# Kernel tuning notes

Hardware: AMD Instinct MI355X
Metric: run time of the kernel (lower is better)

Reference implementation:

```python
import jax, jax.numpy as jnp
import numpy as np

B, F, NP, DIM, H, DH = 4, 16, 196, 512, 8, 64  # batch, frames, patches, dim, heads, dim_head
N = 1 + F * NP  # sequence length incl CLS


def setup_inputs() -> dict:
    key = jax.random.key(0)
    k1, k2, k3, k4 = jax.random.split(key, 4)
    return {
        "x": jax.random.normal(k1, (B, N, DIM), dtype=jnp.float32),
        "W_qkv": jax.random.normal(k2, (DIM, 3 * H * DH), dtype=jnp.float32) * 0.05,
        "W_out": jax.random.normal(k3, (H * DH, DIM), dtype=jnp.float32) * 0.05,
        "b_out": jax.random.normal(k4, (DIM,), dtype=jnp.float32) * 0.05,
        "f": F,
    }


def _attn(q, k, v):
    # q: [bb, i, d], k/v: [bb, j, d]
    sim = jnp.einsum('bid,bjd->bij', q, k)
    a = jax.nn.softmax(sim, axis=-1)
    return jnp.einsum('bij,bjd->bid', a, v)


def reference(x, W_qkv, W_out, b_out, f):
    b, n_tot, dim = x.shape
    h, d = H, DH
    scale = d ** (-0.5)
    qkv = x @ W_qkv  # [b, N, 3*h*d]
    q, k, v = jnp.split(qkv, 3, axis=-1)

    def to_bh(t):  # b n (h d) -> (b h) n d
        return t.reshape(b, n_tot, h, d).transpose(0, 2, 1, 3).reshape(b * h, n_tot, d)

    q, k, v = map(to_bh, (q, k, v))
    q = q * scale

    cls_q, q_ = q[:, :1], q[:, 1:]
    cls_k, k_ = k[:, :1], k[:, 1:]
    cls_v, v_ = v[:, :1], v[:, 1:]

    # CLS token attends over the full sequence
    cls_out = _attn(cls_q, k, v)  # [(b h), 1, d]

    # spatial factorization: (b h) (f n) d -> (b h f) n d
    n = (n_tot - 1) // f
    def split_f(t):
        return t.reshape(b * h * f, n, d)
    q_, k_, v_ = map(split_f, (q_, k_, v_))

    # repeat CLS k/v per frame: b () d -> (b r) () d with r = f
    cls_k_r = jnp.repeat(cls_k, f, axis=0)
    cls_v_r = jnp.repeat(cls_v, f, axis=0)
    k_ = jnp.concatenate([cls_k_r, k_], axis=1)  # [(b h f), n+1, d]
    v_ = jnp.concatenate([cls_v_r, v_], axis=1)

    out = _attn(q_, k_, v_)  # [(b h f), n, d]
    out = out.reshape(b * h, f * n, d)
    out = jnp.concatenate([cls_out, out], axis=1)  # [(b h), N, d]
    out = out.reshape(b, h, n_tot, d).transpose(0, 2, 1, 3).reshape(b, n_tot, h * d)
    return out @ W_out + b_out
```

## Files before the change

kernel.cpp:

```cpp
#include <hip/hip_runtime.h>
#include <math.h>

#define B_   4
#define F_   16
#define NP_  196
#define DIM_ 512
#define H_   8
#define DH_  64
#define NTOT 3137
#define BH_  32
#define MROWS 12548
#define QSZ_ ((size_t)BH_ * NTOT * DH_)
#define KVPAD 224
#define PSTRIDE 232
#define NCHUNK 13

typedef unsigned short u16;
typedef __attribute__((ext_vector_type(8))) short    bf16x8;
typedef __attribute__((ext_vector_type(8))) unsigned short u16x8;
typedef __attribute__((ext_vector_type(4))) unsigned short u16x4;
typedef __attribute__((ext_vector_type(4))) float    f32x4;

__device__ __forceinline__ u16 f2bf(float f) {
    unsigned int u = __float_as_uint(f);
    unsigned int r = (u + 0x7FFFu + ((u >> 16) & 1u)) >> 16;
    return (u16)r;
}
__device__ __forceinline__ float bf2f(u16 u) {
    return __uint_as_float(((unsigned int)u) << 16);
}

__device__ __forceinline__ void gl2lds16(const u16* g, u16* l) {
    __builtin_amdgcn_global_load_lds(
        (const __attribute__((address_space(1))) unsigned int*)(g),
        (__attribute__((address_space(3))) unsigned int*)(l),
        16, 0, 0);
}

__global__ __launch_bounds__(256) void convert_x_kernel(
    const float* __restrict__ x, u16* __restrict__ xbf)
{
    int idx = blockIdx.x * 256 + threadIdx.x;
    float4 v = ((const float4*)x)[idx];
    u16x4 p = { f2bf(v.x), f2bf(v.y), f2bf(v.z), f2bf(v.w) };
    *(u16x4*)(&xbf[(size_t)idx * 4]) = p;
}

__global__ __launch_bounds__(256) void transpose_bf16_kernel(
    const float* __restrict__ src, u16* __restrict__ dst, int R, int C)
{
    __shared__ float t[32][33];
    const int tx = threadIdx.x & 31, ty = threadIdx.x >> 5;
    const int c0 = blockIdx.x * 32, r0 = blockIdx.y * 32;
    #pragma unroll
    for (int i = 0; i < 4; ++i) {
        int r = ty + i * 8;
        t[r][tx] = src[(size_t)(r0 + r) * C + c0 + tx];
    }
    __syncthreads();
    #pragma unroll
    for (int i = 0; i < 4; ++i) {
        int cc = ty + i * 8;
        dst[(size_t)(c0 + cc) * R + r0 + tx] = f2bf(t[tx][cc]);
    }
}

template<int MODE>
__global__ __launch_bounds__(256) void gemm_bf16_mfma(
    const u16* __restrict__ A, const u16* __restrict__ BT,
    u16* __restrict__ Cq, u16* __restrict__ Ck, u16* __restrict__ Cv,
    u16* __restrict__ CvT, float* __restrict__ Cout, const float* __restrict__ bias)
{
    __shared__ alignas(16) u16 Asm[8 * 512];
    __shared__ alignas(16) u16 Bsm[8 * 512];

    const int tid  = threadIdx.x;
    const int wave = tid >> 6, lane = tid & 63;
    const int wr = wave >> 1, wc = wave & 1;
    const int lm = lane & 15, lq = lane >> 4;
    const int row0 = blockIdx.y * 128;
    const int col0 = blockIdx.x * 128;

    f32x4 acc[4][4];
    #pragma unroll
    for (int i = 0; i < 4; ++i)
        #pragma unroll
        for (int j = 0; j < 4; ++j) acc[i][j] = (f32x4){0.f, 0.f, 0.f, 0.f};

    for (int k0 = 0; k0 < 512; k0 += 32) {
        #pragma unroll
        for (int i = 0; i < 2; ++i) {
            int s = wave * 2 + i;
            int arow = row0 + s * 16 + lm;
            if (arow >= MROWS) arow = MROWS - 1;
            gl2lds16(A + (size_t)arow * 512 + k0 + lq * 8, &Asm[s * 512 + lane * 8]);
            int brow = col0 + s * 16 + lm;
            gl2lds16(BT + (size_t)brow * 512 + k0 + lq * 8, &Bsm[s * 512 + lane * 8]);
        }
        __syncthreads();
        bf16x8 af[4], bf[4];
        #pragma unroll
        for (int mi = 0; mi < 4; ++mi)
            af[mi] = *(const bf16x8*)(&Asm[(wr * 4 + mi) * 512 + lane * 8]);
        #pragma unroll
        for (int ni = 0; ni < 4; ++ni)
            bf[ni] = *(const bf16x8*)(&Bsm[(wc * 4 + ni) * 512 + lane * 8]);
        #pragma unroll
        for (int mi = 0; mi < 4; ++mi)
            #pragma unroll
            for (int ni = 0; ni < 4; ++ni)
                acc[mi][ni] = __builtin_amdgcn_mfma_f32_16x16x32_bf16(
                    af[mi], bf[ni], acc[mi][ni], 0, 0, 0);
        __syncthreads();
    }

    if (MODE == 0) {
        const int t3 = col0 >> 9;
        #pragma unroll
        for (int mi = 0; mi < 4; ++mi) {
            #pragma unroll
            for (int r = 0; r < 4; ++r) {
                int gr = row0 + wr * 64 + mi * 16 + lq * 4 + r;
                if (gr >= MROWS) continue;
                int b = gr / NTOT;
                int n = gr - b * NTOT;
                #pragma unroll
                for (int ni = 0; ni < 4; ++ni) {
                    int gc = col0 + wc * 64 + ni * 16 + lm;
                    int rem = gc & 511;
                    int h = rem >> 6, d = rem & 63;
                    int bh = b * H_ + h;
                    size_t tok = (size_t)bh * NTOT + n;
                    float v = acc[mi][ni][r];
                    if (t3 == 0) {
                        Cq[tok * 64 + d] = f2bf(v * 0.125f);
                    } else if (t3 == 1) {
                        Ck[tok * 64 + d] = f2bf(v);
                    } else {
                        u16 bv = f2bf(v);
                        Cv[tok * 64 + d] = bv;
                        if (n > 0) {
                            unsigned nn = (unsigned)(n - 1);
                            unsigned f = nn / 196u;
                            unsigned jj = nn - f * 196u + 1u;
                            CvT[((size_t)(bh * 16 + (int)f) * 64 + d) * KVPAD + jj] = bv;
                        }
                    }
                }
            }
        }
    } else {
        float bb[4];
        #pragma unroll
        for (int ni = 0; ni < 4; ++ni)
            bb[ni] = bias[col0 + wc * 64 + ni * 16 + lm];
        #pragma unroll
        for (int mi = 0; mi < 4; ++mi) {
            #pragma unroll
            for (int r = 0; r < 4; ++r) {
                int gr = row0 + wr * 64 + mi * 16 + lq * 4 + r;
                if (gr >= MROWS) continue;
                #pragma unroll
                for (int ni = 0; ni < 4; ++ni) {
                    int gc = col0 + wc * 64 + ni * 16 + lm;
                    Cout[(size_t)gr * 512 + gc] = acc[mi][ni][r] + bb[ni];
                }
            }
        }
    }
}

__global__ __launch_bounds__(64) void vt_cls_fill_kernel(
    const u16* __restrict__ vb, u16* __restrict__ vT)
{
    const int bh = blockIdx.x, d = threadIdx.x;
    u16 val = vb[(size_t)bh * NTOT * 64 + d];
    #pragma unroll
    for (int f = 0; f < 16; ++f)
        vT[((size_t)(bh * 16 + f) * 64 + d) * KVPAD] = val;
}

__global__ __launch_bounds__(256) void attn_mfma_kernel(
    const u16* __restrict__ qb, const u16* __restrict__ kb,
    const u16* __restrict__ vT, u16* __restrict__ attn)
{
    __shared__ alignas(16) u16 Pbuf[4 * 16 * PSTRIDE];

    const int tid  = threadIdx.x;
    const int wave = tid >> 6, lane = tid & 63;
    const int lm = lane & 15, lq = lane >> 4;
    const int task = blockIdx.x * 4 + wave;
    const int mt = task % 13;
    const int gf = task / 13;
    const int f  = gf & 15;
    const int bh = gf >> 4;

    const int rq = min(mt * 16 + lm, 195);
    const u16* qrow = qb + ((size_t)bh * NTOT + (1 + f * NP_ + rq)) * 64;
    bf16x8 qf0 = *(const bf16x8*)(qrow + lq * 8);
    bf16x8 qf1 = *(const bf16x8*)(qrow + 32 + lq * 8);

    f32x4 S[13];
    #pragma unroll
    for (int nt = 0; nt < 13; ++nt) {
        int rkc = min(nt * 16 + lm, 196);
        int nk = (rkc == 0) ? 0 : (1 + f * NP_ + rkc - 1);
        const u16* krow = kb + ((size_t)bh * NTOT + nk) * 64;
        bf16x8 kf0 = *(const bf16x8*)(krow + lq * 8);
        bf16x8 kf1 = *(const bf16x8*)(krow + 32 + lq * 8);
        f32x4 z = (f32x4){0.f, 0.f, 0.f, 0.f};
        z = __builtin_amdgcn_mfma_f32_16x16x32_bf16(qf0, kf0, z, 0, 0, 0);
        z = __builtin_amdgcn_mfma_f32_16x16x32_bf16(qf1, kf1, z, 0, 0, 0);
        S[nt] = z;
    }

    #pragma unroll
    for (int nt = 0; nt < 13; ++nt)
        if (nt * 16 + lm >= 197) {
            S[nt][0] = -INFINITY; S[nt][1] = -INFINITY;
            S[nt][2] = -INFINITY; S[nt][3] = -INFINITY;
        }

    float invl[4];
    #pragma unroll
    for (int r = 0; r < 4; ++r) {
        float mx = -INFINITY;
        #pragma unroll
        for (int nt = 0; nt < 13; ++nt) mx = fmaxf(mx, S[nt][r]);
        mx = fmaxf(mx, __shfl_xor(mx, 1, 64));
        mx = fmaxf(mx, __shfl_xor(mx, 2, 64));
        mx = fmaxf(mx, __shfl_xor(mx, 4, 64));
        mx = fmaxf(mx, __shfl_xor(mx, 8, 64));
        float sum = 0.f;
        #pragma unroll
        for (int nt = 0; nt < 13; ++nt) {
            float p = __expf(S[nt][r] - mx);
            S[nt][r] = p;
            sum += p;
        }
        sum += __shfl_xor(sum, 1, 64);
        sum += __shfl_xor(sum, 2, 64);
        sum += __shfl_xor(sum, 4, 64);
        sum += __shfl_xor(sum, 8, 64);
        invl[r] = 1.f / sum;
    }

    u16* P = Pbuf + wave * 16 * PSTRIDE;
    #pragma unroll
    for (int nt = 0; nt < 13; ++nt) {
        int col = nt * 16 + lm;
        #pragma unroll
        for (int r = 0; r < 4; ++r)
            P[(lq * 4 + r) * PSTRIDE + col] = f2bf(S[nt][r]);
    }
    {
        u16x4 z4 = {0, 0, 0, 0};
        *(u16x4*)(P + lm * PSTRIDE + 208 + lq * 4) = z4;
    }

    f32x4 O[4];
    #pragma unroll
    for (int nd = 0; nd < 4; ++nd) O[nd] = (f32x4){0.f, 0.f, 0.f, 0.f};
    const u16* vbase = vT + (size_t)(bh * 16 + f) * 64 * KVPAD;
    #pragma unroll
    for (int ks = 0; ks < 7; ++ks) {
        bf16x8 pf = *(const bf16x8*)(P + lm * PSTRIDE + ks * 32 + lq * 8);
        #pragma unroll
        for (int nd = 0; nd < 4; ++nd) {
            bf16x8 vf = *(const bf16x8*)(vbase + (size_t)(nd * 16 + lm) * KVPAD + ks * 32 + lq * 8);
            O[nd] = __builtin_amdgcn_mfma_f32_16x16x32_bf16(pf, vf, O[nd], 0, 0, 0);
        }
    }

    const int b = bh >> 3, h = bh & 7;
    #pragma unroll
    for (int r = 0; r < 4; ++r) {
        int rql = mt * 16 + lq * 4 + r;
        if (rql >= 196) continue;
        int n = 1 + f * NP_ + rql;
        u16* dst = attn + ((size_t)b * NTOT + n) * 512 + h * 64;
        float s = invl[r];
        #pragma unroll
        for (int nd = 0; nd < 4; ++nd)
            dst[nd * 16 + lm] = f2bf(O[nd][r] * s);
    }
}

__global__ __launch_bounds__(256) void attn_cls_partial_kernel(
    const u16* __restrict__ qb, const u16* __restrict__ kb,
    const u16* __restrict__ vb, float* __restrict__ cls_m,
    float* __restrict__ cls_l, float* __restrict__ cls_o)
{
    __shared__ float qs[64];
    __shared__ float redm[4], redl[4];
    __shared__ float ps[256];
    __shared__ float so[4][64];

    const int c = blockIdx.x, bh = blockIdx.y;
    const int t = threadIdx.x;
    const int lane = t & 63, w = t >> 6;

    if (t < 64) qs[t] = bf2f(qb[(size_t)bh * NTOT * 64 + t]);
    __syncthreads();

    const int j = c * 256 + t;
    const bool valid = (j < NTOT);
    const int jc = valid ? j : (NTOT - 1);
    const u16* krow = kb + ((size_t)bh * NTOT + jc) * 64;
    float s0 = 0.f, s1 = 0.f, s2 = 0.f, s3 = 0.f;
    #pragma unroll
    for (int i = 0; i < 8; ++i) {
        u16x8 k8 = *(const u16x8*)(krow + i * 8);
        const float* qp = qs + i * 8;
        s0 = fmaf(qp[0], bf2f(k8[0]), s0);
        s1 = fmaf(qp[1], bf2f(k8[1]), s1);
        s2 = fmaf(qp[2], bf2f(k8[2]), s2);
        s3 = fmaf(qp[3], bf2f(k8[3]), s3);
        s0 = fmaf(qp[4], bf2f(k8[4]), s0);
        s1 = fmaf(qp[5], bf2f(k8[5]), s1);
        s2 = fmaf(qp[6], bf2f(k8[6]), s2);
        s3 = fmaf(qp[7], bf2f(k8[7]), s3);
    }
    float s = (s0 + s1) + (s2 + s3);
    if (!valid) s = -INFINITY;

    float mx = s;
    #pragma unroll
    for (int off = 1; off < 64; off <<= 1) mx = fmaxf(mx, __shfl_xor(mx, off, 64));
    if (lane == 0) redm[w] = mx;
    __syncthreads();
    mx = fmaxf(fmaxf(redm[0], redm[1]), fmaxf(redm[2], redm[3]));

    float pv = __expf(s - mx);
    float l = pv;
    #pragma unroll
    for (int off = 1; off < 64; off <<= 1) l += __shfl_xor(l, off, 64);
    if (lane == 0) redl[w] = l;
    ps[t] = pv;
    __syncthreads();
    l = redl[0] + redl[1] + redl[2] + redl[3];

    const int d = lane, part = w;
    float o = 0.f;
    #pragma unroll 8
    for (int i = 0; i < 64; ++i) {
        int jj = c * 256 + part * 64 + i;
        int jjc = (jj < NTOT) ? jj : (NTOT - 1);
        o = fmaf(ps[part * 64 + i], bf2f(vb[((size_t)bh * NTOT + jjc) * 64 + d]), o);
    }
    so[part][d] = o;
    __syncthreads();
    if (t < 64) {
        float O = so[0][t] + so[1][t] + so[2][t] + so[3][t];
        int pi = bh * NCHUNK + c;
        cls_o[(size_t)pi * 64 + t] = O;
        if (t == 0) { cls_m[pi] = mx; cls_l[pi] = l; }
    }
}

__global__ __launch_bounds__(64) void attn_cls_merge_kernel(
    const float* __restrict__ cls_m, const float* __restrict__ cls_l,
    const float* __restrict__ cls_o, u16* __restrict__ attn)
{
    const int bh = blockIdx.x, lane = threadIdx.x;
    float M = -INFINITY;
    #pragma unroll
    for (int p = 0; p < NCHUNK; ++p) M = fmaxf(M, cls_m[bh * NCHUNK + p]);
    float L = 0.f, O = 0.f;
    #pragma unroll
    for (int p = 0; p < NCHUNK; ++p) {
        float al = __expf(cls_m[bh * NCHUNK + p] - M);
        L += cls_l[bh * NCHUNK + p] * al;
        O += cls_o[(size_t)(bh * NCHUNK + p) * 64 + lane] * al;
    }
    const int b = bh >> 3, h = bh & 7;
    attn[(size_t)b * NTOT * 512 + h * 64 + lane] = f2bf(O / L);
}

extern "C" void kernel_launch(void* const* d_in, const int* in_sizes, int n_in,
                              void* d_out, int out_size, void* d_ws, size_t ws_size,
                              hipStream_t stream) {
    const float* x    = (const float*)d_in[0];
    const float* wqkv = (const float*)d_in[1];
    const float* wout = (const float*)d_in[2];
    const float* bout = (const float*)d_in[3];

    u16* p = (u16*)d_ws;
    u16* xbf   = p;                    p += (size_t)MROWS * 512;
    u16* attn  = xbf;
    u16* wqkvT = p;                    p += (size_t)1536 * 512;
    u16* woutT = p;                    p += (size_t)512 * 512;
    u16* qbuf  = p;                    p += QSZ_;
    u16* kbuf  = p;                    p += QSZ_;
    u16* vbuf  = p;                    p += QSZ_;
    u16* vT    = p;                    p += (size_t)BH_ * 16 * 64 * KVPAD;
    float* clsws = (float*)p;
    float* cls_m = clsws;
    float* cls_l = clsws + BH_ * NCHUNK;
    float* cls_o = clsws + 2 * BH_ * NCHUNK;
    float* outp  = (float*)d_out;

    convert_x_kernel<<<6274, 256, 0, stream>>>(x, xbf);
    transpose_bf16_kernel<<<dim3(48, 16), 256, 0, stream>>>(wqkv, wqkvT, 512, 1536);
    transpose_bf16_kernel<<<dim3(16, 16), 256, 0, stream>>>(wout, woutT, 512, 512);
    gemm_bf16_mfma<0><<<dim3(12, 99), 256, 0, stream>>>(
        xbf, wqkvT, qbuf, kbuf, vbuf, vT, nullptr, nullptr);
    vt_cls_fill_kernel<<<32, 64, 0, stream>>>(vbuf, vT);
    attn_mfma_kernel<<<1664, 256, 0, stream>>>(qbuf, kbuf, vT, attn);
    attn_cls_partial_kernel<<<dim3(NCHUNK, 32), 256, 0, stream>>>(
        qbuf, kbuf, vbuf, cls_m, cls_l, cls_o);
    attn_cls_merge_kernel<<<32, 64, 0, stream>>>(cls_m, cls_l, cls_o, attn);
    gemm_bf16_mfma<1><<<dim3(4, 99), 256, 0, stream>>>(
        attn, woutT, nullptr, nullptr, nullptr, nullptr, outp, bout);
}
```

Measured before the change: 227.3 us.

## Double-buffer GEMM LDS staging, enlarge QKV tile, build transposed V separately

```diff
diff --git a/kernel.cpp b/kernel.cpp
--- a/kernel.cpp
+++ b/kernel.cpp
@@ -65,62 +65,72 @@
     }
 }
 
-template<int MODE>
-__global__ __launch_bounds__(256) void gemm_bf16_mfma(
+template<int MODE, int MI>
+__global__ __launch_bounds__(256, 2) void gemm_bf16_mfma(
     const u16* __restrict__ A, const u16* __restrict__ BT,
     u16* __restrict__ Cq, u16* __restrict__ Ck, u16* __restrict__ Cv,
-    u16* __restrict__ CvT, float* __restrict__ Cout, const float* __restrict__ bias)
-{
-    __shared__ alignas(16) u16 Asm[8 * 512];
-    __shared__ alignas(16) u16 Bsm[8 * 512];
+    float* __restrict__ Cout, const float* __restrict__ bias)
+{
+    constexpr int ASUB = MI * 2;
+    __shared__ alignas(16) u16 Asm[2][ASUB * 512];
+    __shared__ alignas(16) u16 Bsm[2][8 * 512];
 
     const int tid  = threadIdx.x;
     const int wave = tid >> 6, lane = tid & 63;
     const int wr = wave >> 1, wc = wave & 1;
     const int lm = lane & 15, lq = lane >> 4;
-    const int row0 = blockIdx.y * 128;
+    const int row0 = blockIdx.y * (MI * 32);
     const int col0 = blockIdx.x * 128;
 
-    f32x4 acc[4][4];
-    #pragma unroll
-    for (int i = 0; i < 4; ++i)
+    f32x4 acc[MI][4];
+    #pragma unroll
+    for (int i = 0; i < MI; ++i)
         #pragma unroll
         for (int j = 0; j < 4; ++j) acc[i][j] = (f32x4){0.f, 0.f, 0.f, 0.f};
 
-    for (int k0 = 0; k0 < 512; k0 += 32) {
+    auto stage = [&](int k0, int buf) {
+        #pragma unroll
+        for (int i = 0; i < ASUB / 4; ++i) {
+            int s = wave * (ASUB / 4) + i;
+            int arow = row0 + s * 16 + lm;
+            if (arow >= MROWS) arow = MROWS - 1;
+            gl2lds16(A + (size_t)arow * 512 + k0 + lq * 8, &Asm[buf][s * 512 + lane * 8]);
+        }
         #pragma unroll
         for (int i = 0; i < 2; ++i) {
             int s = wave * 2 + i;
-            int arow = row0 + s * 16 + lm;
-            if (arow >= MROWS) arow = MROWS - 1;
-            gl2lds16(A + (size_t)arow * 512 + k0 + lq * 8, &Asm[s * 512 + lane * 8]);
             int brow = col0 + s * 16 + lm;
-            gl2lds16(BT + (size_t)brow * 512 + k0 + lq * 8, &Bsm[s * 512 + lane * 8]);
-        }
+            gl2lds16(BT + (size_t)brow * 512 + k0 + lq * 8, &Bsm[buf][s * 512 + lane * 8]);
+        }
+    };
+
+    stage(0, 0);
+    for (int it = 0; it < 16; ++it) {
         __syncthreads();
-        bf16x8 af[4], bf[4];
-        #pragma unroll
-        for (int mi = 0; mi < 4; ++mi)
-            af[mi] = *(const bf16x8*)(&Asm[(wr * 4 + mi) * 512 + lane * 8]);
+        if (it < 15) stage((it + 1) * 32, (it + 1) & 1);
+        const int buf = it & 1;
+        bf16x8 af[MI], bf[4];
+        #pragma unroll
+        for (int mi = 0; mi < MI; ++mi)
+            af[mi] = *(const bf16x8*)(&Asm[buf][(wr * MI + mi) * 512 + lane * 8]);
         #pragma unroll
         for (int ni = 0; ni < 4; ++ni)
-            bf[ni] = *(const bf16x8*)(&Bsm[(wc * 4 + ni) * 512 + lane * 8]);
-        #pragma unroll
-        for (int mi = 0; mi < 4; ++mi)
+            bf[ni] = *(const bf16x8*)(&Bsm[buf][(wc * 4 + ni) * 512 + lane * 8]);
+        #pragma unroll
+        for (int mi = 0; mi < MI; ++mi)
             #pragma unroll
             for (int ni = 0; ni < 4; ++ni)
                 acc[mi][ni] = __builtin_amdgcn_mfma_f32_16x16x32_bf16(
                     af[mi], bf[ni], acc[mi][ni], 0, 0, 0);
-        __syncthreads();
     }
 
     if (MODE == 0) {
         const int t3 = col0 >> 9;
         #pragma unroll
-        for (int mi = 0; mi < 4; ++mi) {
+        for (int mi = 0; mi < MI; ++mi) {
             #pragma unroll
             for (int r = 0; r < 4; ++r) {
-                int gr = row0 + wr * 64 + mi * 16 + lq * 4 + r;
+                int gr = row0 + wr * (MI * 16) + mi * 16 + lq * 4 + r;
                 if (gr >= MROWS) continue;
                 int b = gr / NTOT;
                 int n = gr - b * NTOT;
@@ -129,23 +139,11 @@
                     int gc = col0 + wc * 64 + ni * 16 + lm;
                     int rem = gc & 511;
                     int h = rem >> 6, d = rem & 63;
-                    int bh = b * H_ + h;
-                    size_t tok = (size_t)bh * NTOT + n;
+                    size_t tok = (size_t)(b * H_ + h) * NTOT + n;
                     float v = acc[mi][ni][r];
-                    if (t3 == 0) {
-                        Cq[tok * 64 + d] = f2bf(v * 0.125f);
-                    } else if (t3 == 1) {
-                        Ck[tok * 64 + d] = f2bf(v);
-                    } else {
-                        u16 bv = f2bf(v);
-                        Cv[tok * 64 + d] = bv;
-                        if (n > 0) {
-                            unsigned nn = (unsigned)(n - 1);
-                            unsigned f = nn / 196u;
-                            unsigned jj = nn - f * 196u + 1u;
-                            CvT[((size_t)(bh * 16 + (int)f) * 64 + d) * KVPAD + jj] = bv;
-                        }
-                    }
+                    if (t3 == 0)      Cq[tok * 64 + d] = f2bf(v * 0.125f);
+                    else if (t3 == 1) Ck[tok * 64 + d] = f2bf(v);
+                    else              Cv[tok * 64 + d] = f2bf(v);
                 }
             }
         }
@@ -155,10 +153,10 @@
         for (int ni = 0; ni < 4; ++ni)
             bb[ni] = bias[col0 + wc * 64 + ni * 16 + lm];
         #pragma unroll
-        for (int mi = 0; mi < 4; ++mi) {
+        for (int mi = 0; mi < MI; ++mi) {
             #pragma unroll
             for (int r = 0; r < 4; ++r) {
-                int gr = row0 + wr * 64 + mi * 16 + lq * 4 + r;
+                int gr = row0 + wr * (MI * 16) + mi * 16 + lq * 4 + r;
                 if (gr >= MROWS) continue;
                 #pragma unroll
                 for (int ni = 0; ni < 4; ++ni) {
@@ -170,14 +168,24 @@
     }
 }
 
-__global__ __launch_bounds__(64) void vt_cls_fill_kernel(
+__global__ __launch_bounds__(256) void vt_build_kernel(
     const u16* __restrict__ vb, u16* __restrict__ vT)
 {
-    const int bh = blockIdx.x, d = threadIdx.x;
-    u16 val = vb[(size_t)bh * NTOT * 64 + d];
-    #pragma unroll
-    for (int f = 0; f < 16; ++f)
-        vT[((size_t)(bh * 16 + f) * 64 + d) * KVPAD] = val;
+    const int g = blockIdx.x;
+    const int bh = g >> 4, f = g & 15;
+    const int d = threadIdx.x & 63, jq = threadIdx.x >> 6;
+    const int j0 = blockIdx.y * 32;
+    u16* dst = vT + ((size_t)g * 64 + d) * KVPAD;
+    #pragma unroll
+    for (int i = 0; i < 8; ++i) {
+        int jj = j0 + i * 4 + jq;
+        u16 val = 0;
+        if (jj <= 196) {
+            int n = (jj == 0) ? 0 : (1 + f * NP_ + jj - 1);
+            val = vb[((size_t)bh * NTOT + n) * 64 + d];
+        }
+        dst[jj] = val;
+    }
 }
 
 __global__ __launch_bounds__(256) void attn_mfma_kernel(
@@ -403,13 +411,13 @@
     convert_x_kernel<<<6274, 256, 0, stream>>>(x, xbf);
     transpose_bf16_kernel<<<dim3(48, 16), 256, 0, stream>>>(wqkv, wqkvT, 512, 1536);
     transpose_bf16_kernel<<<dim3(16, 16), 256, 0, stream>>>(wout, woutT, 512, 512);
-    gemm_bf16_mfma<0><<<dim3(12, 99), 256, 0, stream>>>(
-        xbf, wqkvT, qbuf, kbuf, vbuf, vT, nullptr, nullptr);
-    vt_cls_fill_kernel<<<32, 64, 0, stream>>>(vbuf, vT);
+    gemm_bf16_mfma<0, 8><<<dim3(12, 50), 256, 0, stream>>>(
+        xbf, wqkvT, qbuf, kbuf, vbuf, nullptr, nullptr);
+    vt_build_kernel<<<dim3(512, 7), 256, 0, stream>>>(vbuf, vT);
     attn_mfma_kernel<<<1664, 256, 0, stream>>>(qbuf, kbuf, vT, attn);
     attn_cls_partial_kernel<<<dim3(NCHUNK, 32), 256, 0, stream>>>(
         qbuf, kbuf, vbuf, cls_m, cls_l, cls_o);
     attn_cls_merge_kernel<<<32, 64, 0, stream>>>(cls_m, cls_l, cls_o, attn);
-    gemm_bf16_mfma<1><<<dim3(4, 99), 256, 0, stream>>>(
-        attn, woutT, nullptr, nullptr, nullptr, nullptr, outp, bout);
-}
+    gemm_bf16_mfma<1, 4><<<dim3(4, 99), 256, 0, stream>>>(
+        attn, woutT, nullptr, nullptr, nullptr, outp, bout);
+}
```

After: 268.7 us. +18.2%, slower.
